# Kernel tuning notes

Measured on AMD Instinct MI355X. Metric: run time of the kernel, lower is better.

The kernel has to match this reference:

```python
import jax, jax.numpy as jnp
import numpy as np

EMBED = 1024
HEADS = 16
HEAD_DIM = EMBED // HEADS          # 64
POS_DIM = 256
POS_PER_HEAD = POS_DIM // HEADS    # 16
POS_IDX = 64
N, L = 8, 1024


def setup_inputs() -> dict:
    key = jax.random.key(0)
    ks = jax.random.split(key, 10)
    s = 0.02
    return {
        "values": jax.random.normal(ks[0], (N, L, EMBED), jnp.float32),
        "keys": jax.random.normal(ks[1], (N, L, EMBED), jnp.float32),
        "query": jax.random.normal(ks[2], (N, L, EMBED), jnp.float32),
        "position": jax.random.normal(ks[3], (N, L, POS_IDX), jnp.float32),
        # torch Linear weights: shape (out_features, in_features)
        "Wv": jax.random.normal(ks[4], (HEAD_DIM, HEAD_DIM), jnp.float32) * s,
        "Wk": jax.random.normal(ks[5], (HEAD_DIM, HEAD_DIM), jnp.float32) * s,
        "Wq": jax.random.normal(ks[6], (HEAD_DIM, HEAD_DIM + POS_PER_HEAD), jnp.float32) * s,
        "Wpos": jax.random.normal(ks[7], (POS_DIM, POS_IDX), jnp.float32) * s,
        "Wo": jax.random.normal(ks[8], (EMBED, EMBED), jnp.float32) * s,
        "bo": jax.random.normal(ks[9], (EMBED,), jnp.float32) * s,
    }


def reference(values, keys, query, position, Wv, Wk, Wq, Wpos, Wo, bo):
    n, qlen = query.shape[0], query.shape[1]
    vlen, klen = values.shape[1], keys.shape[1]
    # position embedding: Linear(pos_idx -> pos_dim)
    pos_emb = position @ Wpos.T                                   # [N, q, POS_DIM]
    q_with_pos = jnp.concatenate([query, pos_emb], axis=2)        # [N, q, EMBED+POS_DIM]
    # split heads
    v = values.reshape(n, vlen, HEADS, HEAD_DIM)
    k = keys.reshape(n, klen, HEADS, HEAD_DIM)
    qp = q_with_pos.reshape(n, qlen, HEADS, HEAD_DIM + POS_PER_HEAD)
    # per-head linear projections (no bias)
    v = jnp.einsum('nlhd,ed->nlhe', v, Wv)
    k = jnp.einsum('nlhd,ed->nlhe', k, Wk)
    q = jnp.einsum('nqhd,ed->nqhe', qp, Wq)
    # attention: note scale uses sqrt(embed_size), as in the original
    energy = jnp.einsum('nqhd,nkhd->nhqk', q, k)
    attn = jax.nn.softmax(energy / jnp.sqrt(jnp.asarray(EMBED, energy.dtype)), axis=3)
    out = jnp.einsum('nhql,nlhd->nqhd', attn, v).reshape(n, qlen, EMBED)
    return out @ Wo.T + bo
```

## Files before the change

### kernel.cpp

```cpp
#include <hip/hip_runtime.h>
#include <hip/hip_bf16.h>


typedef __hip_bfloat16 bf16;
typedef unsigned int u32;
typedef unsigned short u16;
typedef short short8 __attribute__((ext_vector_type(8)));
typedef float f32x4 __attribute__((ext_vector_type(4)));
typedef float f32x16 __attribute__((ext_vector_type(16)));
typedef unsigned int u32x2 __attribute__((ext_vector_type(2)));

#define MFMA16(a, b, c) __builtin_amdgcn_mfma_f32_16x16x32_bf16((a), (b), (c), 0, 0, 0)
#define MFMA32(a, b, c) __builtin_amdgcn_mfma_f32_32x32x16_bf16((a), (b), (c), 0, 0, 0)

#define QSCALE 0.04508422002777998f

__device__ __forceinline__ short8 ld8(const bf16* p) { return *(const short8*)p; }

__device__ __forceinline__ u32 pk2(float a, float b) {
  u16 ua = __bfloat16_as_ushort(__float2bfloat16(a));
  u16 ub = __bfloat16_as_ushort(__float2bfloat16(b));
  return (u32)ua | ((u32)ub << 16);
}

__device__ __forceinline__ float fexp2(float x) {
  float r;
  asm("v_exp_f32 %0, %1" : "=v"(r) : "v"(x));
  return r;
}

__device__ __forceinline__ u32 cvtpk(float a, float b) {
  u32 r;
  asm("v_cvt_pk_bf16_f32 %0, %1, %2" : "=v"(r) : "v"(a), "v"(b));
  return r;
}

__device__ __forceinline__ void gload16(const void* g, void* l) {
  __builtin_amdgcn_global_load_lds(
      (const __attribute__((address_space(1))) u32*)g,
      (__attribute__((address_space(3))) u32*)l, 16, 0, 0);
}

union S8U { short8 s; u32 u[4]; };

__device__ __forceinline__ short8 ld8f(const float* p) {
  float4 a = ((const float4*)p)[0];
  float4 b = ((const float4*)p)[1];
  S8U r;
  r.u[0] = pk2(a.x, a.y);
  r.u[1] = pk2(a.z, a.w);
  r.u[2] = pk2(b.x, b.y);
  r.u[3] = pk2(b.z, b.w);
  return r.s;
}

__global__ __launch_bounds__(256) void cvt_wo(const float* __restrict__ w,
                                              bf16* __restrict__ o) {
  int i = blockIdx.x * 256 + threadIdx.x;
  o[i] = __float2bfloat16(w[i]);
}

__global__ __launch_bounds__(256) void pos_gemm(const float* __restrict__ position,
                                                const float* __restrict__ Wpos,
                                                bf16* __restrict__ posb) {
  const int t = threadIdx.x;
  const int lane = t & 63, wave = t >> 6;
  const int g = lane >> 4, c = lane & 15;
  const int wr = wave >> 1, wc = wave & 1;
  const int r0 = blockIdx.x * 128 + wr * 64;
  const int c0 = blockIdx.y * 128 + wc * 64;
  f32x4 acc[4][4];
#pragma unroll
  for (int ai = 0; ai < 4; ++ai)
#pragma unroll
    for (int bi = 0; bi < 4; ++bi) acc[ai][bi] = (f32x4){0.f, 0.f, 0.f, 0.f};
#pragma unroll
  for (int k0 = 0; k0 < 64; k0 += 32) {
    short8 af[4], bfr[4];
#pragma unroll
    for (int ai = 0; ai < 4; ++ai)
      af[ai] = ld8f(position + (size_t)(r0 + ai * 16 + c) * 64 + k0 + 8 * g);
#pragma unroll
    for (int bi = 0; bi < 4; ++bi)
      bfr[bi] = ld8f(Wpos + (size_t)(c0 + bi * 16 + c) * 64 + k0 + 8 * g);
#pragma unroll
    for (int ai = 0; ai < 4; ++ai)
#pragma unroll
      for (int bi = 0; bi < 4; ++bi) acc[ai][bi] = MFMA16(af[ai], bfr[bi], acc[ai][bi]);
  }
#pragma unroll
  for (int bi = 0; bi < 4; ++bi) {
    const int p = c0 + bi * 16 + c;
#pragma unroll
    for (int ai = 0; ai < 4; ++ai) {
#pragma unroll
      for (int i = 0; i < 4; ++i) {
        int row = r0 + ai * 16 + 4 * g + i;
        posb[(size_t)row * 256 + p] = __float2bfloat16(acc[ai][bi][i]);
      }
    }
  }
}

__global__ __launch_bounds__(256) void k_gemm(const float* __restrict__ src,
                                              const float* __restrict__ W,
                                              bf16* __restrict__ dst) {
  const int t = threadIdx.x;
  const int lane = t & 63, wave = t >> 6;
  const int g = lane >> 4, c = lane & 15;
  const int wr = wave >> 1, wc = wave & 1;
  const int r0 = blockIdx.x * 128 + wr * 64;
  const int c0 = wc * 32;
  const int h = blockIdx.y;
  f32x4 acc[4][2];
#pragma unroll
  for (int ai = 0; ai < 4; ++ai)
#pragma unroll
    for (int bi = 0; bi < 2; ++bi) acc[ai][bi] = (f32x4){0.f, 0.f, 0.f, 0.f};
#pragma unroll
  for (int k0 = 0; k0 < 64; k0 += 32) {
    short8 af[4], bfr[2];
#pragma unroll
    for (int ai = 0; ai < 4; ++ai)
      af[ai] = ld8f(src + (size_t)(r0 + ai * 16 + c) * 1024 + 64 * h + k0 + 8 * g);
#pragma unroll
    for (int bi = 0; bi < 2; ++bi)
      bfr[bi] = ld8f(W + (size_t)(c0 + bi * 16 + c) * 64 + k0 + 8 * g);
#pragma unroll
    for (int ai = 0; ai < 4; ++ai)
#pragma unroll
      for (int bi = 0; bi < 2; ++bi) acc[ai][bi] = MFMA16(af[ai], bfr[bi], acc[ai][bi]);
  }
#pragma unroll
  for (int bi = 0; bi < 2; ++bi) {
    const int e = c0 + bi * 16 + c;
#pragma unroll
    for (int ai = 0; ai < 4; ++ai) {
#pragma unroll
      for (int i = 0; i < 4; ++i) {
        int row = r0 + ai * 16 + 4 * g + i;
        int n = row >> 10, l = row & 1023;
        dst[(((size_t)(n * 16 + h)) * 1024 + l) * 64 + e] = __float2bfloat16(acc[ai][bi][i]);
      }
    }
  }
}

__global__ __launch_bounds__(256) void v_gemm(const float* __restrict__ src,
                                              const float* __restrict__ W,
                                              bf16* __restrict__ vT) {
  __shared__ __align__(16) char tlds[64 * 272];
  const int t = threadIdx.x;
  const int lane = t & 63, wave = t >> 6;
  const int g = lane >> 4, c = lane & 15;
  const int wr = wave >> 1, wc = wave & 1;
  const int r0 = blockIdx.x * 128 + wr * 64;
  const int c0 = wc * 32;
  const int h = blockIdx.y;
  f32x4 acc[4][2];
#pragma unroll
  for (int ai = 0; ai < 4; ++ai)
#pragma unroll
    for (int bi = 0; bi < 2; ++bi) acc[ai][bi] = (f32x4){0.f, 0.f, 0.f, 0.f};
#pragma unroll
  for (int k0 = 0; k0 < 64; k0 += 32) {
    short8 af[4], bfr[2];
#pragma unroll
    for (int ai = 0; ai < 4; ++ai)
      af[ai] = ld8f(src + (size_t)(r0 + ai * 16 + c) * 1024 + 64 * h + k0 + 8 * g);
#pragma unroll
    for (int bi = 0; bi < 2; ++bi)
      bfr[bi] = ld8f(W + (size_t)(c0 + bi * 16 + c) * 64 + k0 + 8 * g);
#pragma unroll
    for (int ai = 0; ai < 4; ++ai)
#pragma unroll
      for (int bi = 0; bi < 2; ++bi) acc[ai][bi] = MFMA16(af[ai], bfr[bi], acc[ai][bi]);
  }
#pragma unroll
  for (int bi = 0; bi < 2; ++bi) {
    const int e_loc = c0 + bi * 16 + c;
#pragma unroll
    for (int ai = 0; ai < 4; ++ai) {
      const int l0 = wr * 64 + ai * 16 + 4 * g;
      *(u32*)(tlds + e_loc * 272 + l0 * 2) = pk2(acc[ai][bi][0], acc[ai][bi][1]);
      *(u32*)(tlds + e_loc * 272 + l0 * 2 + 4) = pk2(acc[ai][bi][2], acc[ai][bi][3]);
    }
  }
  __syncthreads();
  const int n = blockIdx.x >> 3;
  const int lglob0 = (blockIdx.x & 7) * 128;
  bf16* vbase = vT + ((size_t)(n * 16 + h)) * 64 * 1024;
#pragma unroll
  for (int j = 0; j < 4; ++j) {
    const int id = t + j * 256;
    const int e = id >> 4, lc = (id & 15) * 8;
    *(short8*)(vbase + (size_t)e * 1024 + lglob0 + lc) =
        *(const short8*)(tlds + e * 272 + lc * 2);
  }
}

__global__ __launch_bounds__(256) void q_gemm(const float* __restrict__ query,
                                              const bf16* __restrict__ posb,
                                              const float* __restrict__ Wq,
                                              bf16* __restrict__ qb) {
  const int t = threadIdx.x;
  const int lane = t & 63, wave = t >> 6;
  const int g = lane >> 4, c = lane & 15;
  const int wr = wave >> 1, wc = wave & 1;
  const int r0 = blockIdx.x * 128 + wr * 64;
  const int c0 = wc * 32;
  const int h = blockIdx.y;
  f32x4 acc[4][2];
#pragma unroll
  for (int ai = 0; ai < 4; ++ai)
#pragma unroll
    for (int bi = 0; bi < 2; ++bi) acc[ai][bi] = (f32x4){0.f, 0.f, 0.f, 0.f};
  const short8 z8 = (short8){0, 0, 0, 0, 0, 0, 0, 0};
#pragma unroll
  for (int k0 = 0; k0 < 80; k0 += 32) {
    const bool tail_dead = (k0 == 64) && (g >= 2);
    const int col = 80 * h + k0 + 8 * g;
    short8 af[4], bfr[2];
#pragma unroll
    for (int ai = 0; ai < 4; ++ai) {
      const int row = r0 + ai * 16 + c;
      af[ai] = tail_dead ? z8
               : (col < 1024 ? ld8f(query + (size_t)row * 1024 + col)
                             : ld8(posb + (size_t)row * 256 + (col - 1024)));
    }
#pragma unroll
    for (int bi = 0; bi < 2; ++bi)
      bfr[bi] = tail_dead ? z8
                          : ld8f(Wq + (size_t)(c0 + bi * 16 + c) * 80 + k0 + 8 * g);
#pragma unroll
    for (int ai = 0; ai < 4; ++ai)
#pragma unroll
      for (int bi = 0; bi < 2; ++bi) acc[ai][bi] = MFMA16(af[ai], bfr[bi], acc[ai][bi]);
  }
#pragma unroll
  for (int bi = 0; bi < 2; ++bi) {
    const int e = c0 + bi * 16 + c;
#pragma unroll
    for (int ai = 0; ai < 4; ++ai) {
#pragma unroll
      for (int i = 0; i < 4; ++i) {
        int row = r0 + ai * 16 + 4 * g + i;
        int n = row >> 10, l = row & 1023;
        qb[(((size_t)(n * 16 + h)) * 1024 + l) * 64 + e] =
            __float2bfloat16(acc[ai][bi][i] * QSCALE);
      }
    }
  }
}

__global__ __launch_bounds__(256, 2) void attn_kernel(const bf16* __restrict__ qb,
                                                      const bf16* __restrict__ kb,
                                                      const bf16* __restrict__ vT,
                                                      bf16* __restrict__ ob) {
  __shared__ __align__(16) char smem[2][16384];
  const int t = threadIdx.x;
  const int lane = t & 63, wave = t >> 6;
  const int l31 = lane & 31, hi = lane >> 5;
  const int qt = blockIdx.x, h = blockIdx.y, n = blockIdx.z;
  const int nh = n * 16 + h;
  const int q0 = qt * 256 + wave * 64;

  const bf16* kpan = kb + (size_t)nh * 65536;
  const bf16* vpan = vT + (size_t)nh * 65536;

  const int sr8 = lane >> 3;
  const int scg = (lane & 7) ^ sr8;
  const int row0 = wave * 8 + sr8;
  const bf16* kgA = kpan + (size_t)row0 * 64 + scg * 8;
  const bf16* kgB = kpan + (size_t)(32 + row0) * 64 + scg * 8;
  const bf16* vgA = vpan + (size_t)row0 * 1024 + scg * 8;
  const bf16* vgB = vpan + (size_t)(32 + row0) * 1024 + scg * 8;
  const int ldsoff = wave * 1024;

  const bf16* qrowA = qb + ((size_t)nh * 1024 + q0 + l31) * 64 + 8 * hi;
  const bf16* qrowB = qrowA + 32 * 64;
  short8 qfA[4], qfB[4];
#pragma unroll
  for (int ds = 0; ds < 4; ++ds) {
    qfA[ds] = ld8(qrowA + ds * 16);
    qfB[ds] = ld8(qrowB + ds * 16);
  }

  f32x16 accA0, accA1, accB0, accB1;
#pragma unroll
  for (int r = 0; r < 16; ++r) {
    accA0[r] = 0.f;
    accA1[r] = 0.f;
    accB0[r] = 0.f;
    accB1[r] = 0.f;
  }
  float lA = 0.f, lB = 0.f;

  gload16(kgA, smem[0] + ldsoff);
  gload16(kgB, smem[0] + 4096 + ldsoff);
  gload16(vgA, smem[0] + 8192 + ldsoff);
  gload16(vgB, smem[0] + 12288 + ldsoff);
  __syncthreads();

  int cur = 0;
  for (int kt = 0; kt < 16; ++kt) {
    if (kt < 15) {
      char* sn = smem[cur ^ 1];
      const size_t ko = (size_t)(kt + 1) * 4096;
      const int vo = (kt + 1) * 64;
      gload16(kgA + ko, sn + ldsoff);
      gload16(kgB + ko, sn + 4096 + ldsoff);
      gload16(vgA + vo, sn + 8192 + ldsoff);
      gload16(vgB + vo, sn + 12288 + ldsoff);
    }
    const char* kt_ = smem[cur];
    const char* vt_ = smem[cur] + 8192;

#pragma unroll
    for (int s = 0; s < 2; ++s) {
      const int kr = s * 32 + l31;
      short8 kf[4], vf[2][2];
#pragma unroll
      for (int ds = 0; ds < 4; ++ds)
        kf[ds] = *(const short8*)(kt_ + kr * 128 + (((2 * ds + hi) ^ (kr & 7)) << 4));
#pragma unroll
      for (int dt = 0; dt < 2; ++dt) {
        const int vr = dt * 32 + l31;
#pragma unroll
        for (int ks = 0; ks < 2; ++ks)
          vf[dt][ks] = *(const short8*)(
              vt_ + vr * 128 + (((s * 4 + ks * 2 + hi) ^ (vr & 7)) << 4));
      }

      f32x16 srA, srB;
#pragma unroll
      for (int r = 0; r < 16; ++r) {
        srA[r] = 0.f;
        srB[r] = 0.f;
      }
      __builtin_amdgcn_s_setprio(1);
      srA = MFMA32(kf[0], qfA[0], srA);
      srA = MFMA32(kf[1], qfA[1], srA);
      srA = MFMA32(kf[2], qfA[2], srA);
      srA = MFMA32(kf[3], qfA[3], srA);
      srB = MFMA32(kf[0], qfB[0], srB);
      srB = MFMA32(kf[1], qfB[1], srB);
      srB = MFMA32(kf[2], qfB[2], srB);
      srB = MFMA32(kf[3], qfB[3], srB);
      __builtin_amdgcn_s_setprio(0);

      float pA[16], pB[16];
#pragma unroll
      for (int r = 0; r < 16; ++r) pA[r] = fexp2(srA[r]);
#pragma unroll
      for (int r = 0; r < 16; ++r) pB[r] = fexp2(srB[r]);

      u32 a01 = cvtpk(pA[0], pA[1]), a23 = cvtpk(pA[2], pA[3]);
      u32 a45 = cvtpk(pA[4], pA[5]), a67 = cvtpk(pA[6], pA[7]);
      u32 a89 = cvtpk(pA[8], pA[9]), aab = cvtpk(pA[10], pA[11]);
      u32 acd = cvtpk(pA[12], pA[13]), aef = cvtpk(pA[14], pA[15]);
      u32x2 sa0 = __builtin_amdgcn_permlane32_swap(a01, a45, false, false);
      u32x2 sa1 = __builtin_amdgcn_permlane32_swap(a23, a67, false, false);
      u32x2 sa2 = __builtin_amdgcn_permlane32_swap(a89, acd, false, false);
      u32x2 sa3 = __builtin_amdgcn_permlane32_swap(aab, aef, false, false);
      S8U pfA0, pfA1;
      pfA0.u[0] = sa0[0];
      pfA0.u[1] = sa1[0];
      pfA0.u[2] = sa0[1];
      pfA0.u[3] = sa1[1];
      pfA1.u[0] = sa2[0];
      pfA1.u[1] = sa3[0];
      pfA1.u[2] = sa2[1];
      pfA1.u[3] = sa3[1];

      u32 b01 = cvtpk(pB[0], pB[1]), b23 = cvtpk(pB[2], pB[3]);
      u32 b45 = cvtpk(pB[4], pB[5]), b67 = cvtpk(pB[6], pB[7]);
      u32 b89 = cvtpk(pB[8], pB[9]), bab = cvtpk(pB[10], pB[11]);
      u32 bcd = cvtpk(pB[12], pB[13]), bef = cvtpk(pB[14], pB[15]);
      u32x2 sb0 = __builtin_amdgcn_permlane32_swap(b01, b45, false, false);
      u32x2 sb1 = __builtin_amdgcn_permlane32_swap(b23, b67, false, false);
      u32x2 sb2 = __builtin_amdgcn_permlane32_swap(b89, bcd, false, false);
      u32x2 sb3 = __builtin_amdgcn_permlane32_swap(bab, bef, false, false);
      S8U pfB0, pfB1;
      pfB0.u[0] = sb0[0];
      pfB0.u[1] = sb1[0];
      pfB0.u[2] = sb0[1];
      pfB0.u[3] = sb1[1];
      pfB1.u[0] = sb2[0];
      pfB1.u[1] = sb3[0];
      pfB1.u[2] = sb2[1];
      pfB1.u[3] = sb3[1];

      __builtin_amdgcn_s_setprio(1);
      accA0 = MFMA32(vf[0][0], pfA0.s, accA0);
      accA0 = MFMA32(vf[0][1], pfA1.s, accA0);
      accA1 = MFMA32(vf[1][0], pfA0.s, accA1);
      accA1 = MFMA32(vf[1][1], pfA1.s, accA1);
      accB0 = MFMA32(vf[0][0], pfB0.s, accB0);
      accB0 = MFMA32(vf[0][1], pfB1.s, accB0);
      accB1 = MFMA32(vf[1][0], pfB0.s, accB1);
      accB1 = MFMA32(vf[1][1], pfB1.s, accB1);
      __builtin_amdgcn_s_setprio(0);

      float psA = ((pA[0] + pA[1]) + (pA[2] + pA[3])) +
                  ((pA[4] + pA[5]) + (pA[6] + pA[7])) +
                  ((pA[8] + pA[9]) + (pA[10] + pA[11])) +
                  ((pA[12] + pA[13]) + (pA[14] + pA[15]));
      float psB = ((pB[0] + pB[1]) + (pB[2] + pB[3])) +
                  ((pB[4] + pB[5]) + (pB[6] + pB[7])) +
                  ((pB[8] + pB[9]) + (pB[10] + pB[11])) +
                  ((pB[12] + pB[13]) + (pB[14] + pB[15]));
      psA += __shfl_xor(psA, 32);
      psB += __shfl_xor(psB, 32);
      lA += psA;
      lB += psB;
    }
    __syncthreads();
    cur ^= 1;
  }

  const float invA = 1.f / lA, invB = 1.f / lB;
  bf16* obaseA = ob + ((size_t)(n * 1024 + q0 + l31) * 16 + h) * 64;
  bf16* obaseB = obaseA + (size_t)32 * 16 * 64;
#pragma unroll
  for (int dt = 0; dt < 2; ++dt) {
#pragma unroll
    for (int rb = 0; rb < 4; ++rb) {
      const int d0 = dt * 32 + rb * 8 + 4 * hi;
      const f32x16& aA = dt ? accA1 : accA0;
      const f32x16& aB = dt ? accB1 : accB0;
      u32x2 wA, wB;
      wA[0] = pk2(aA[4 * rb + 0] * invA, aA[4 * rb + 1] * invA);
      wA[1] = pk2(aA[4 * rb + 2] * invA, aA[4 * rb + 3] * invA);
      wB[0] = pk2(aB[4 * rb + 0] * invB, aB[4 * rb + 1] * invB);
      wB[1] = pk2(aB[4 * rb + 2] * invB, aB[4 * rb + 3] * invB);
      *(u32x2*)(obaseA + d0) = wA;
      *(u32x2*)(obaseB + d0) = wB;
    }
  }
}

__global__ __launch_bounds__(256) void out_gemm(const bf16* __restrict__ A,
                                                const bf16* __restrict__ B,
                                                const float* __restrict__ bias,
                                                float* __restrict__ out) {
  __shared__ __align__(16) char smem[2][16384];
  const int t = threadIdx.x;
  const int lane = t & 63, wave = t >> 6;
  const int g = lane >> 4, c = lane & 15;
  const int wr = wave >> 1, wc = wave & 1;
  const int r0 = blockIdx.y * 128;
  const int c0 = blockIdx.x * 128;

  const int srow = t >> 2;
  const int scg = (t & 3) ^ ((srow >> 1) & 3);
  const bf16* ag0 = A + (size_t)(r0 + srow) * 1024 + scg * 8;
  const bf16* ag1 = A + (size_t)(r0 + 64 + srow) * 1024 + scg * 8;
  const bf16* bg0 = B + (size_t)(c0 + srow) * 1024 + scg * 8;
  const bf16* bg1 = B + (size_t)(c0 + 64 + srow) * 1024 + scg * 8;

  f32x4 acc[4][4];
#pragma unroll
  for (int ai = 0; ai < 4; ++ai)
#pragma unroll
    for (int bi = 0; bi < 4; ++bi) acc[ai][bi] = (f32x4){0.f, 0.f, 0.f, 0.f};

  const int wb = wave * 1024;

  {
    char* s0 = smem[0];
    gload16(ag0, s0 + wb);
    gload16(ag1, s0 + 4096 + wb);
    gload16(bg0, s0 + 8192 + wb);
    gload16(bg1, s0 + 12288 + wb);
  }
  __syncthreads();

  int cur = 0;
  for (int kt = 0; kt < 32; ++kt) {
    if (kt < 31) {
      const int k1 = (kt + 1) * 32;
      char* sn = smem[cur ^ 1];
      gload16(ag0 + k1, sn + wb);
      gload16(ag1 + k1, sn + 4096 + wb);
      gload16(bg0 + k1, sn + 8192 + wb);
      gload16(bg1 + k1, sn + 12288 + wb);
    }
    const char* sa = smem[cur];
    const char* sb = smem[cur] + 8192;

    short8 af[4], bfr[4];
#pragma unroll
    for (int ai = 0; ai < 4; ++ai) {
      const int row = wr * 64 + ai * 16 + c;
      af[ai] = *(const short8*)(sa + row * 64 + ((g ^ ((row >> 1) & 3)) << 4));
    }
#pragma unroll
    for (int bi = 0; bi < 4; ++bi) {
      const int row = wc * 64 + bi * 16 + c;
      bfr[bi] = *(const short8*)(sb + row * 64 + ((g ^ ((row >> 1) & 3)) << 4));
    }
    __builtin_amdgcn_s_setprio(1);
#pragma unroll
    for (int ai = 0; ai < 4; ++ai)
#pragma unroll
      for (int bi = 0; bi < 4; ++bi) acc[ai][bi] = MFMA16(af[ai], bfr[bi], acc[ai][bi]);
    __builtin_amdgcn_s_setprio(0);

    __syncthreads();
    cur ^= 1;
  }

#pragma unroll
  for (int bi = 0; bi < 4; ++bi) {
    const int e = c0 + wc * 64 + bi * 16 + c;
    const float bv = bias[e];
#pragma unroll
    for (int ai = 0; ai < 4; ++ai) {
#pragma unroll
      for (int i = 0; i < 4; ++i) {
        out[(size_t)(r0 + wr * 64 + ai * 16 + 4 * g + i) * 1024 + e] =
            acc[ai][bi][i] + bv;
      }
    }
  }
}

extern "C" void kernel_launch(void* const* d_in, const int* in_sizes, int n_in,
                              void* d_out, int out_size, void* d_ws, size_t ws_size,
                              hipStream_t stream) {
  const float* values = (const float*)d_in[0];
  const float* keys = (const float*)d_in[1];
  const float* query = (const float*)d_in[2];
  const float* position = (const float*)d_in[3];
  const float* Wv = (const float*)d_in[4];
  const float* Wk = (const float*)d_in[5];
  const float* Wq = (const float*)d_in[6];
  const float* Wpos = (const float*)d_in[7];
  const float* Wo = (const float*)d_in[8];
  const float* bo = (const float*)d_in[9];

  char* ws = (char*)d_ws;
  bf16* qb = (bf16*)(ws);
  bf16* kb = (bf16*)(ws + ((size_t)16 << 20));
  bf16* vT = (bf16*)(ws + ((size_t)32 << 20));
  bf16* posb = (bf16*)(ws + ((size_t)48 << 20));
  bf16* ob = (bf16*)(ws + ((size_t)52 << 20));
  bf16* wo16 = (bf16*)(ws + ((size_t)68 << 20));
  float* out = (float*)d_out;

  cvt_wo<<<4096, 256, 0, stream>>>(Wo, wo16);
  pos_gemm<<<dim3(64, 2), 256, 0, stream>>>(position, Wpos, posb);
  k_gemm<<<dim3(64, 16), 256, 0, stream>>>(keys, Wk, kb);
  v_gemm<<<dim3(64, 16), 256, 0, stream>>>(values, Wv, vT);
  q_gemm<<<dim3(64, 16), 256, 0, stream>>>(query, posb, Wq, qb);
  attn_kernel<<<dim3(4, 16, 8), 256, 0, stream>>>(qb, kb, vT, ob);
  out_gemm<<<dim3(8, 64), 256, 0, stream>>>(ob, wo16, bo, out);
}
```

Measured before the change: 132.5 us.

## Halve attention block size to 128 threads and remap blocks across XCDs

The attention kernel now runs 2 waves per block over 128 query rows, doubling the grid to 1024 blocks. A 1D block index is swizzled so consecutive blocks go to different XCDs while blocks sharing a head's K/V panel are grouped together. K/V tile loads are redone so two waves fill the whole 64-row tile in four strided chunks. The aim is better CU fill and L2 locality, at the cost of K/V tiles being loaded twice as often in total.

```diff
diff --git a/kernel.cpp b/kernel.cpp
--- a/kernel.cpp
+++ b/kernel.cpp
@@ -253,7 +253,7 @@
   }
 }
 
-__global__ __launch_bounds__(256, 2) void attn_kernel(const bf16* __restrict__ qb,
+__global__ __launch_bounds__(128, 4) void attn_kernel(const bf16* __restrict__ qb,
                                                       const bf16* __restrict__ kb,
                                                       const bf16* __restrict__ vT,
                                                       bf16* __restrict__ ob) {
@@ -261,9 +261,11 @@
   const int t = threadIdx.x;
   const int lane = t & 63, wave = t >> 6;
   const int l31 = lane & 31, hi = lane >> 5;
-  const int qt = blockIdx.x, h = blockIdx.y, n = blockIdx.z;
+  const int bid = blockIdx.x;
+  const int w = (bid & 7) * 128 + (bid >> 3);
+  const int qt = w & 7, h = (w >> 3) & 15, n = w >> 7;
   const int nh = n * 16 + h;
-  const int q0 = qt * 256 + wave * 64;
+  const int q0 = qt * 128 + wave * 64;
 
   const bf16* kpan = kb + (size_t)nh * 65536;
   const bf16* vpan = vT + (size_t)nh * 65536;
@@ -271,10 +273,8 @@
   const int sr8 = lane >> 3;
   const int scg = (lane & 7) ^ sr8;
   const int row0 = wave * 8 + sr8;
-  const bf16* kgA = kpan + (size_t)row0 * 64 + scg * 8;
-  const bf16* kgB = kpan + (size_t)(32 + row0) * 64 + scg * 8;
-  const bf16* vgA = vpan + (size_t)row0 * 1024 + scg * 8;
-  const bf16* vgB = vpan + (size_t)(32 + row0) * 1024 + scg * 8;
+  const bf16* kg = kpan + (size_t)row0 * 64 + scg * 8;
+  const bf16* vg = vpan + (size_t)row0 * 1024 + scg * 8;
   const int ldsoff = wave * 1024;
 
   const bf16* qrowA = qb + ((size_t)nh * 1024 + q0 + l31) * 64 + 8 * hi;
@@ -296,22 +296,24 @@
   }
   float lA = 0.f, lB = 0.f;
 
-  gload16(kgA, smem[0] + ldsoff);
-  gload16(kgB, smem[0] + 4096 + ldsoff);
-  gload16(vgA, smem[0] + 8192 + ldsoff);
-  gload16(vgB, smem[0] + 12288 + ldsoff);
+#pragma unroll
+  for (int j = 0; j < 4; ++j) {
+    gload16(kg + (size_t)j * 16 * 64, smem[0] + j * 2048 + ldsoff);
+    gload16(vg + (size_t)j * 16 * 1024, smem[0] + 8192 + j * 2048 + ldsoff);
+  }
   __syncthreads();
 
   int cur = 0;
   for (int kt = 0; kt < 16; ++kt) {
     if (kt < 15) {
       char* sn = smem[cur ^ 1];
-      const size_t ko = (size_t)(kt + 1) * 4096;
-      const int vo = (kt + 1) * 64;
-      gload16(kgA + ko, sn + ldsoff);
-      gload16(kgB + ko, sn + 4096 + ldsoff);
-      gload16(vgA + vo, sn + 8192 + ldsoff);
-      gload16(vgB + vo, sn + 12288 + ldsoff);
+      const bf16* kk = kg + (size_t)(kt + 1) * 4096;
+      const bf16* vv = vg + (kt + 1) * 64;
+#pragma unroll
+      for (int j = 0; j < 4; ++j) {
+        gload16(kk + (size_t)j * 16 * 64, sn + j * 2048 + ldsoff);
+        gload16(vv + (size_t)j * 16 * 1024, sn + 8192 + j * 2048 + ldsoff);
+      }
     }
     const char* kt_ = smem[cur];
     const char* vt_ = smem[cur] + 8192;
@@ -554,6 +556,6 @@
   k_gemm<<<dim3(64, 16), 256, 0, stream>>>(keys, Wk, kb);
   v_gemm<<<dim3(64, 16), 256, 0, stream>>>(values, Wv, vT);
   q_gemm<<<dim3(64, 16), 256, 0, stream>>>(query, posb, Wq, qb);
-  attn_kernel<<<dim3(4, 16, 8), 256, 0, stream>>>(qb, kb, vT, ob);
+  attn_kernel<<<1024, 128, 0, stream>>>(qb, kb, vT, ob);
   out_gemm<<<dim3(8, 64), 256, 0, stream>>>(ob, wo16, bo, out);
 }
```

New measurement: 136.3 us. 1.03x slower.

## Deepen out_gemm K-tile to 64 and remap attention blocks across XCDs

Applied to the files above, without the earlier changes.

The output projection GEMM now stages 64-wide K slices per iteration with a 128-byte-row XOR swizzle. This halves the number of loop iterations and barriers, at the cost of doubling LDS per block to 64 KB. The attention launch becomes a flat 1D grid with a block-index permutation. The permutation places the four query tiles of the same (n, head) on the same XCD (bid&7), so their shared K/V panels can be reused in that XCD's L2.

```diff
diff --git a/kernel.cpp b/kernel.cpp
--- a/kernel.cpp
+++ b/kernel.cpp
@@ -261,7 +261,9 @@
   const int t = threadIdx.x;
   const int lane = t & 63, wave = t >> 6;
   const int l31 = lane & 31, hi = lane >> 5;
-  const int qt = blockIdx.x, h = blockIdx.y, n = blockIdx.z;
+  const int bid = blockIdx.x;
+  const int w = (bid & 7) * 64 + (bid >> 3);
+  const int qt = w & 3, h = (w >> 2) & 15, n = w >> 6;
   const int nh = n * 16 + h;
   const int q0 = qt * 256 + wave * 64;
 
@@ -444,7 +446,7 @@
                                                 const bf16* __restrict__ B,
                                                 const float* __restrict__ bias,
                                                 float* __restrict__ out) {
-  __shared__ __align__(16) char smem[2][16384];
+  __shared__ __align__(16) char smem[2][32768];
   const int t = threadIdx.x;
   const int lane = t & 63, wave = t >> 6;
   const int g = lane >> 4, c = lane & 15;
@@ -452,12 +454,12 @@
   const int r0 = blockIdx.y * 128;
   const int c0 = blockIdx.x * 128;
 
-  const int srow = t >> 2;
-  const int scg = (t & 3) ^ ((srow >> 1) & 3);
-  const bf16* ag0 = A + (size_t)(r0 + srow) * 1024 + scg * 8;
-  const bf16* ag1 = A + (size_t)(r0 + 64 + srow) * 1024 + scg * 8;
-  const bf16* bg0 = B + (size_t)(c0 + srow) * 1024 + scg * 8;
-  const bf16* bg1 = B + (size_t)(c0 + 64 + srow) * 1024 + scg * 8;
+  const int sr8 = lane >> 3;
+  const int scg = (lane & 7) ^ sr8;
+  const int row0 = wave * 8 + sr8;
+  const bf16* ag = A + (size_t)(r0 + row0) * 1024 + scg * 8;
+  const bf16* bg = B + (size_t)(c0 + row0) * 1024 + scg * 8;
+  const int ldsoff = wave * 1024;
 
   f32x4 acc[4][4];
 #pragma unroll
@@ -465,47 +467,47 @@
 #pragma unroll
     for (int bi = 0; bi < 4; ++bi) acc[ai][bi] = (f32x4){0.f, 0.f, 0.f, 0.f};
 
-  const int wb = wave * 1024;
-
-  {
-    char* s0 = smem[0];
-    gload16(ag0, s0 + wb);
-    gload16(ag1, s0 + 4096 + wb);
-    gload16(bg0, s0 + 8192 + wb);
-    gload16(bg1, s0 + 12288 + wb);
+#pragma unroll
+  for (int j = 0; j < 4; ++j) {
+    gload16(ag + (size_t)j * 32 * 1024, smem[0] + j * 4096 + ldsoff);
+    gload16(bg + (size_t)j * 32 * 1024, smem[0] + 16384 + j * 4096 + ldsoff);
   }
   __syncthreads();
 
   int cur = 0;
-  for (int kt = 0; kt < 32; ++kt) {
-    if (kt < 31) {
-      const int k1 = (kt + 1) * 32;
+  for (int kt = 0; kt < 16; ++kt) {
+    if (kt < 15) {
       char* sn = smem[cur ^ 1];
-      gload16(ag0 + k1, sn + wb);
-      gload16(ag1 + k1, sn + 4096 + wb);
-      gload16(bg0 + k1, sn + 8192 + wb);
-      gload16(bg1 + k1, sn + 12288 + wb);
+      const int k1 = (kt + 1) * 64;
+#pragma unroll
+      for (int j = 0; j < 4; ++j) {
+        gload16(ag + (size_t)j * 32 * 1024 + k1, sn + j * 4096 + ldsoff);
+        gload16(bg + (size_t)j * 32 * 1024 + k1, sn + 16384 + j * 4096 + ldsoff);
+      }
     }
     const char* sa = smem[cur];
-    const char* sb = smem[cur] + 8192;
-
-    short8 af[4], bfr[4];
-#pragma unroll
-    for (int ai = 0; ai < 4; ++ai) {
-      const int row = wr * 64 + ai * 16 + c;
-      af[ai] = *(const short8*)(sa + row * 64 + ((g ^ ((row >> 1) & 3)) << 4));
-    }
-#pragma unroll
-    for (int bi = 0; bi < 4; ++bi) {
-      const int row = wc * 64 + bi * 16 + c;
-      bfr[bi] = *(const short8*)(sb + row * 64 + ((g ^ ((row >> 1) & 3)) << 4));
-    }
-    __builtin_amdgcn_s_setprio(1);
-#pragma unroll
-    for (int ai = 0; ai < 4; ++ai)
-#pragma unroll
-      for (int bi = 0; bi < 4; ++bi) acc[ai][bi] = MFMA16(af[ai], bfr[bi], acc[ai][bi]);
-    __builtin_amdgcn_s_setprio(0);
+    const char* sb = smem[cur] + 16384;
+
+#pragma unroll
+    for (int h2 = 0; h2 < 2; ++h2) {
+      short8 af[4], bfr[4];
+#pragma unroll
+      for (int ai = 0; ai < 4; ++ai) {
+        const int row = wr * 64 + ai * 16 + c;
+        af[ai] = *(const short8*)(sa + row * 128 + (((h2 * 4 + g) ^ (row & 7)) << 4));
+      }
+#pragma unroll
+      for (int bi = 0; bi < 4; ++bi) {
+        const int row = wc * 64 + bi * 16 + c;
+        bfr[bi] = *(const short8*)(sb + row * 128 + (((h2 * 4 + g) ^ (row & 7)) << 4));
+      }
+      __builtin_amdgcn_s_setprio(1);
+#pragma unroll
+      for (int ai = 0; ai < 4; ++ai)
+#pragma unroll
+        for (int bi = 0; bi < 4; ++bi) acc[ai][bi] = MFMA16(af[ai], bfr[bi], acc[ai][bi]);
+      __builtin_amdgcn_s_setprio(0);
+    }
 
     __syncthreads();
     cur ^= 1;
@@ -554,6 +556,6 @@
   k_gemm<<<dim3(64, 16), 256, 0, stream>>>(keys, Wk, kb);
   v_gemm<<<dim3(64, 16), 256, 0, stream>>>(values, Wv, vT);
   q_gemm<<<dim3(64, 16), 256, 0, stream>>>(query, posb, Wq, qb);
-  attn_kernel<<<dim3(4, 16, 8), 256, 0, stream>>>(qb, kb, vT, ob);
+  attn_kernel<<<512, 256, 0, stream>>>(qb, kb, vT, ob);
   out_gemm<<<dim3(8, 64), 256, 0, stream>>>(ob, wo16, bo, out);
 }
```

Measured after the change: 129.6 us. -2.2%, faster.
